# Kernel optimization log

Measured on AMD Instinct MI355X. Metric: run time of the kernel, lower is better.

The kernel has to match this reference:

```python
import jax, jax.numpy as jnp
import numpy as np

ALPHA = 0.8          # triple vs qualifier mixing weight (StarE/QUAD 'sum' strategy)
NUM_ENT = 200000
NUM_REL = 100        # base relations; with inverses rel table has 2*NUM_REL rows
E_DIR = 500000       # edges per direction; edge_index has 2*E_DIR columns
NQ_DIR = 400000      # qualifier (rel, ent, edge_id) triples per direction
D = 200              # emb_dim == gcn_dim
B = 4096             # batch of statements
QP = 6               # qualifier pairs per statement -> quals_ix is [B, 2*QP]


def setup_inputs() -> dict:
    key = jax.random.key(0)
    ks = jax.random.split(key, 24)
    f = lambda i, shape: jax.random.normal(ks[i], shape, jnp.float32) * 0.05
    inp = {
        "ent_embs": f(0, (NUM_ENT, D)),
        "rel_embs": f(1, (2 * NUM_REL, D)),
    }
    for j, n in enumerate(["w_in1", "w_out1", "w_loop1", "w_rel1", "w_q1",
                           "w_in2", "w_out2", "w_loop2", "w_rel2", "w_q2"]):
        inp[n] = f(2 + j, (D, D))
    inp["loop_rel1"] = f(12, (1, D))
    inp["loop_rel2"] = f(13, (1, D))
    inp["b1"] = jnp.zeros((D,), jnp.float32)
    inp["b2"] = jnp.zeros((D,), jnp.float32)
    src = jax.random.randint(ks[14], (E_DIR,), 0, NUM_ENT)
    dst = jax.random.randint(ks[15], (E_DIR,), 0, NUM_ENT)
    # second half are inverse edges
    inp["edge_index"] = jnp.concatenate([jnp.stack([src, dst]), jnp.stack([dst, src])], axis=1)
    et = jax.random.randint(ks[16], (E_DIR,), 0, NUM_REL)
    inp["edge_type"] = jnp.concatenate([et, et + NUM_REL])
    q_r = jax.random.randint(ks[17], (2 * NQ_DIR,), 0, 2 * NUM_REL)
    q_e = jax.random.randint(ks[18], (2 * NQ_DIR,), 0, NUM_ENT)
    q_eid = jax.random.randint(ks[19], (2 * NQ_DIR,), 0, E_DIR)
    inp["quals"] = jnp.stack([q_r, q_e, q_eid])  # [3, 2*NQ_DIR]
    inp["ent_ix"] = jax.random.randint(ks[20], (B,), 0, NUM_ENT)
    inp["rel_ix"] = jax.random.randint(ks[21], (B,), 0, 2 * NUM_REL)
    qi_r = jax.random.randint(ks[22], (B, QP), 0, 2 * NUM_REL)
    qi_e = jax.random.randint(ks[23], (B, QP), 0, NUM_ENT)
    inp["quals_ix"] = jnp.stack([qi_r, qi_e], axis=-1).reshape(B, 2 * QP)  # alternating rel, ent
    return inp


def _comp(h, r):  # CompGCN 'mult' composition
    return h * r


def _compgcn_conv(x, r, edge_index, edge_type, quals,
                  w_in, w_out, w_loop, w_rel, w_q, loop_rel, bias):
    n_ent = x.shape[0]
    E = edge_index.shape[1] // 2
    NQ = quals.shape[1] // 2
    rel_all = jnp.concatenate([r, loop_rel], axis=0)  # loop relation appended last

    def one_dir(idx, etype, q_r, q_e, q_eid, w):
        src, dst = idx[0], idx[1]
        # qualifier-aware per-edge relation embedding
        q_msg = _comp(x[q_e], rel_all[q_r])                               # [NQ, d]
        q_agg = jax.ops.segment_sum(q_msg, q_eid, num_segments=E)        # scatter-sum onto edges
        rel_e = ALPHA * rel_all[etype] + (1.0 - ALPHA) * (q_agg @ w_q)   # [E, d]
        msg = _comp(x[src], rel_e) @ w                                   # [E, d_out]
        deg = jax.ops.segment_sum(jnp.ones((E,), x.dtype), src, num_segments=n_ent)
        dinv = jnp.where(deg > 0, jax.lax.rsqrt(jnp.maximum(deg, 1.0)), 0.0)
        norm = dinv[src] * dinv[dst]                                     # sym degree norm
        return jax.ops.segment_sum(norm[:, None] * msg, dst, num_segments=n_ent)

    in_res = one_dir(edge_index[:, :E], edge_type[:E],
                     quals[0, :NQ], quals[1, :NQ], quals[2, :NQ], w_in)
    out_res = one_dir(edge_index[:, E:], edge_type[E:],
                      quals[0, NQ:], quals[1, NQ:], quals[2, NQ:], w_out)
    loop_res = _comp(x, loop_rel) @ w_loop
    out = (in_res + out_res + loop_res) / 3.0 + bias
    return jnp.tanh(out), rel_all[:-1] @ w_rel


def reference(ent_embs, rel_embs,
              w_in1, w_out1, w_loop1, w_rel1, w_q1, loop_rel1, b1,
              w_in2, w_out2, w_loop2, w_rel2, w_q2, loop_rel2, b2,
              edge_index, edge_type, quals, ent_ix, rel_ix, quals_ix):
    x, r = _compgcn_conv(ent_embs, rel_embs, edge_index, edge_type, quals,
                         w_in1, w_out1, w_loop1, w_rel1, w_q1, loop_rel1, b1)
    x, r = _compgcn_conv(x, r, edge_index, edge_type, quals,
                         w_in2, w_out2, w_loop2, w_rel2, w_q2, loop_rel2, b2)
    sub_emb = x[ent_ix]                                   # [B, d]
    rel_emb = r[rel_ix]                                   # [B, d]
    quals_ents = quals_ix[:, 1::2].reshape(-1)
    quals_rels = quals_ix[:, 0::2].reshape(-1)
    qual_obj_emb = x[quals_ents].reshape(sub_emb.shape[0], -1, sub_emb.shape[1])
    qual_rel_emb = r[quals_rels].reshape(rel_emb.shape[0], -1, rel_emb.shape[1])
    return (sub_emb, rel_emb, qual_obj_emb, qual_rel_emb, x, r)
```

## Files before the change

kernel.cpp:

```cpp
#include <hip/hip_runtime.h>
#include <cstdio>


#define ALPHA_MIX 0.8f

constexpr int N_ENT  = 200000;
constexpr int D_     = 200;
constexpr int E_DIR_ = 500000;
constexpr int NQ_    = 400000;
constexpr int B_     = 4096;

constexpr int NT_  = 13;
constexpr int LDA_ = 232;
constexpr int WLD_ = 224;
constexpr int SB_  = 232;
constexpr int PB_  = 80;
constexpr int NTILES_ = (N_ENT + 15) / 16;

constexpr size_t OFS_SUB  = 0;
constexpr size_t OFS_REL  = 819200;
constexpr size_t OFS_QOBJ = 1638400;
constexpr size_t OFS_QREL = 6553600;
constexpr size_t OFS_X    = 11468800;
constexpr size_t OFS_R    = 51468800;

typedef __bf16 bf16x8 __attribute__((ext_vector_type(8)));
typedef float  f32x4  __attribute__((ext_vector_type(4)));

__device__ __forceinline__ unsigned int f2bf(float f) {
  unsigned int u = __float_as_uint(f);
  u += 0x7FFFu + ((u >> 16) & 1u);
  return u >> 16;
}
__device__ __forceinline__ unsigned long long pack4bf(float x, float y, float z, float w) {
  return (unsigned long long)f2bf(x) | ((unsigned long long)f2bf(y) << 16) |
         ((unsigned long long)f2bf(z) << 32) | ((unsigned long long)f2bf(w) << 48);
}
__device__ __forceinline__ float bf_lo(unsigned int u) { return __uint_as_float(u << 16); }
__device__ __forceinline__ float bf_hi(unsigned int u) { return __uint_as_float(u & 0xFFFF0000u); }
__device__ __forceinline__ unsigned int mulpk(unsigned int a, unsigned int b) {
  return f2bf(bf_lo(a) * bf_lo(b)) | (f2bf(bf_hi(a) * bf_hi(b)) << 16);
}
__device__ __forceinline__ float fast_tanh(float x) {
  float xx = fminf(fmaxf(x, -9.0f), 9.0f);
  float e = __builtin_amdgcn_exp2f(xx * 2.8853900817779268f);
  return (e - 1.0f) * __builtin_amdgcn_rcpf(e + 1.0f);
}

typedef short v2s __attribute__((ext_vector_type(2)));
__device__ __forceinline__ void atomic_pk_add_bf16(unsigned short* addr, unsigned int pk) {
#if __has_builtin(__builtin_amdgcn_global_atomic_fadd_v2bf16)
  v2s v;
  __builtin_memcpy(&v, &pk, 4);
  __builtin_amdgcn_global_atomic_fadd_v2bf16(
      (__attribute__((address_space(1))) v2s*)(unsigned long long)addr, v);
#else
  unsigned int* ap = (unsigned int*)addr;
  unsigned int old = *ap;
  while (true) {
    unsigned int nv = f2bf(bf_lo(old) + bf_lo(pk)) | (f2bf(bf_hi(old) + bf_hi(pk)) << 16);
    unsigned int prev = atomicCAS(ap, old, nv);
    if (prev == old) break;
    old = prev;
  }
#endif
}

__global__ __launch_bounds__(256)
void gemm_qual(const unsigned short* __restrict__ Xbf, const unsigned short* __restrict__ Rbf,
               const int* __restrict__ q_e, const int* __restrict__ q_r,
               const int* __restrict__ q_eid,
               const int* __restrict__ srcv, const int* __restrict__ dstv,
               const float* __restrict__ nrm,
               const unsigned short* __restrict__ Bp,
               unsigned short* __restrict__ pre, int nrows)
{
  __shared__ __align__(16) unsigned short As[64 * LDA_];
  __shared__ int s_g[64], s_r[64], s_eid[64], s_dst[64];
  __shared__ float s_nm[64];

  const int t  = threadIdx.x;
  const int r0 = blockIdx.x * 64;

  if (t < 64) {
    int cr = min(r0 + t, nrows - 1);
    s_g[t] = q_e[cr]; s_r[t] = q_r[cr]; s_eid[t] = q_eid[cr];
  }
  __syncthreads();

  for (int task = t; task < 64 * 25; task += 256) {
    int i = task / 25, c = task % 25;
    uint4 xv = ((const uint4*)(Xbf + (size_t)s_g[i] * D_))[c];
    uint4 rv = ((const uint4*)(Rbf + (size_t)s_r[i] * D_))[c];
    uint4 o;
    o.x = mulpk(xv.x, rv.x); o.y = mulpk(xv.y, rv.y);
    o.z = mulpk(xv.z, rv.z); o.w = mulpk(xv.w, rv.w);
    *(uint4*)(As + i * LDA_ + c * 8) = o;
  }
  for (int task = t; task < 64 * 3; task += 256) {
    int i = task / 3, c = task % 3;
    *(uint4*)(As + i * LDA_ + 200 + c * 8) = make_uint4(0, 0, 0, 0);
  }
  __syncthreads();

  const int wave = t >> 6, lane = t & 63;
  const int m = lane & 15, quad = lane >> 4;

  f32x4 acc[NT_];
  const f32x4 zero = {0.f, 0.f, 0.f, 0.f};
  #pragma unroll
  for (int i = 0; i < NT_; i++) acc[i] = zero;

  {
    const unsigned short* arow = As + (wave * 16 + m) * LDA_ + quad * 8;
    const unsigned short* brow = Bp + (size_t)m * WLD_ + quad * 8;
    #pragma unroll
    for (int ks = 0; ks < 7; ks++) {
      bf16x8 av = *(const bf16x8*)(arow + ks * 32);
      #pragma unroll
      for (int tt = 0; tt < NT_; tt++) {
        bf16x8 bv = *(const bf16x8*)(brow + (size_t)tt * 16 * WLD_ + ks * 32);
        acc[tt] = __builtin_amdgcn_mfma_f32_16x16x32_bf16(av, bv, acc[tt], 0, 0, 0);
      }
    }
  }

  __syncthreads();
  if (t < 64) {
    int e = s_eid[t];
    s_dst[t] = dstv[e];
    s_nm[t]  = (1.0f - ALPHA_MIX) * nrm[e];
    s_g[t]   = srcv[e];
  }
  __syncthreads();
  for (int task = t; task < 64 * 25; task += 256) {
    int i = task / 25, c = task % 25;
    *(uint4*)(As + i * LDA_ + c * 8) = ((const uint4*)(Xbf + (size_t)s_g[i] * D_))[c];
  }
  __syncthreads();

  #pragma unroll
  for (int rg = 0; rg < 4; rg++) {
    int row = r0 + wave * 16 + quad * 4 + rg;
    bool valid = row < nrows;
    int li = row - r0;
    size_t orow = (size_t)s_dst[li] * D_;
    float nm = s_nm[li];
    #pragma unroll
    for (int tt = 0; tt < NT_; tt++) {
      int col = tt * 16 + m;
      float xv = (col < D_) ? __uint_as_float(((unsigned int)As[li * LDA_ + col]) << 16) : 0.0f;
      float v  = acc[tt][rg] * nm * xv;
      float vn = __shfl_xor(v, 1);
      if (valid && !(m & 1) && col < D_) {
        unsigned int pk = f2bf(v) | (f2bf(vn) << 16);
        atomic_pk_add_bf16(pre + orow + col, pk);
      }
    }
  }
}

__global__ __launch_bounds__(256)
void node_gather(const int* __restrict__ starts, const int* __restrict__ csr,
                 const int* __restrict__ srcv, const int* __restrict__ et,
                 const float* __restrict__ nrm,
                 const unsigned short* __restrict__ xbf,
                 const unsigned short* __restrict__ rallbf,
                 unsigned short* __restrict__ pre)
{
  int node = blockIdx.x * 4 + (threadIdx.x >> 6);
  if (node >= N_ENT) return;
  int lane = threadIdx.x & 63;
  int p0 = starts[node], p1 = starts[node + 1];
  float a0 = 0.f, a1 = 0.f, a2 = 0.f, a3 = 0.f;
  for (int p = p0; p < p1; p++) {
    int e = csr[p];
    int s = srcv[e], ty = et[e];
    float nm = nrm[e];
    if (lane < 50) {
      uint2 xv = ((const uint2*)(xbf + (size_t)s * D_))[lane];
      uint2 rv = ((const uint2*)(rallbf + (size_t)ty * D_))[lane];
      a0 += nm * bf_lo(xv.x) * bf_lo(rv.x);
      a1 += nm * bf_hi(xv.x) * bf_hi(rv.x);
      a2 += nm * bf_lo(xv.y) * bf_lo(rv.y);
      a3 += nm * bf_hi(xv.y) * bf_hi(rv.y);
    }
  }
  if (lane < 50) {
    uint2 o;
    o.x = f2bf(a0 * ALPHA_MIX) | (f2bf(a1 * ALPHA_MIX) << 16);
    o.y = f2bf(a2 * ALPHA_MIX) | (f2bf(a3 * ALPHA_MIX) << 16);
    ((uint2*)(pre + (size_t)node * D_))[lane] = o;
  }
}

template<int NTH>
__device__ __forceinline__ void node_core(
    const unsigned short* Bl,
    const unsigned short* __restrict__ pre0,
    const unsigned short* __restrict__ pre1,
    const unsigned short* __restrict__ xsrc,
    const uint4* lv,
    const float* __restrict__ bias,
    float* __restrict__ xo, unsigned short* __restrict__ xbo,
    int rowblk, int wave, int m, int quad, int ncol0, int nrows)
{
  for (int i = wave; i < 49; i += 8) {
    int T = rowblk * 49 + i;
    if (T >= NTILES_) break;
    int rowi = min(T * 16 + m, nrows - 1);
    const unsigned short* a0 = pre0 + (size_t)rowi * D_ + quad * 8;
    const unsigned short* a1 = pre1 + (size_t)rowi * D_ + quad * 8;
    const unsigned short* a2 = xsrc + (size_t)rowi * D_ + quad * 8;

    uint4 af[3][7];
    #pragma unroll
    for (int ks = 0; ks < 7; ks++) af[0][ks] = *(const uint4*)(a0 + ks * 32);
    #pragma unroll
    for (int ks = 0; ks < 7; ks++) af[1][ks] = *(const uint4*)(a1 + ks * 32);
    #pragma unroll
    for (int ks = 0; ks < 7; ks++) af[2][ks] = *(const uint4*)(a2 + ks * 32);

    f32x4 acc[NTH];
    const f32x4 zero = {0.f, 0.f, 0.f, 0.f};
    #pragma unroll
    for (int tt = 0; tt < NTH; tt++) acc[tt] = zero;

    #pragma unroll
    for (int seg = 0; seg < 3; seg++) {
      #pragma unroll
      for (int ks = 0; ks < 7; ks++) {
        uint4 a = af[seg][ks];
        if (seg == 2) {
          a.x = mulpk(a.x, lv[ks].x); a.y = mulpk(a.y, lv[ks].y);
          a.z = mulpk(a.z, lv[ks].z); a.w = mulpk(a.w, lv[ks].w);
        }
        bf16x8 av; __builtin_memcpy(&av, &a, 16);
        #pragma unroll
        for (int tt = 0; tt < NTH; tt++) {
          const unsigned short* bp = Bl + (size_t)(seg * PB_ + tt * 16 + m) * SB_ + quad * 8 + ks * 32;
          bf16x8 bv = *(const bf16x8*)bp;
          acc[tt] = __builtin_amdgcn_mfma_f32_16x16x32_bf16(av, bv, acc[tt], 0, 0, 0);
        }
      }
    }

    #pragma unroll
    for (int rg = 0; rg < 4; rg++) {
      int row = T * 16 + quad * 4 + rg;
      if (row < nrows) {
        #pragma unroll
        for (int tt = 0; tt < NTH; tt++) {
          int col = ncol0 + tt * 16 + m;
          if (col < D_) {
            float v = acc[tt][rg] * (1.0f / 3.0f) + bias[col];
            float th = fast_tanh(v);
            if (xo)  xo[(size_t)row * D_ + col] = th;
            if (xbo) xbo[(size_t)row * D_ + col] = (unsigned short)f2bf(th);
          }
        }
      }
    }
  }
}

__global__ __launch_bounds__(512)
void gemm_node(const unsigned short* __restrict__ pre0,
               const unsigned short* __restrict__ pre1,
               const unsigned short* __restrict__ xsrc,
               const unsigned short* __restrict__ lrel,
               const unsigned short* __restrict__ B0,
               const unsigned short* __restrict__ B1,
               const unsigned short* __restrict__ B2,
               const float* __restrict__ bias,
               float* __restrict__ xo, unsigned short* __restrict__ xbo,
               int nrows)
{
  __shared__ __align__(16) unsigned short Bl[3 * PB_ * SB_];
  const int t   = threadIdx.x;
  const int bid = blockIdx.x;
  const int x8 = bid & 7, q = bid >> 3;
  const int part   = q % 3;
  const int rowblk = (q / 3) * 8 + x8;
  const int nth    = (part == 2) ? 3 : 5;
  const int ncol0  = part * PB_;
  const int nrB    = nth * 16;

  const unsigned short* Bs[3] = {B0, B1, B2};
  for (int task = t; task < 3 * nrB * 28; task += 512) {
    int seg = task / (nrB * 28);
    int rem = task % (nrB * 28);
    int n = rem / 28, c = rem % 28;
    uint4 v = *(const uint4*)(Bs[seg] + (size_t)(ncol0 + n) * WLD_ + c * 8);
    *(uint4*)(Bl + (size_t)(seg * PB_ + n) * SB_ + c * 8) = v;
  }
  __syncthreads();

  const int wave = t >> 6, lane = t & 63;
  const int m = lane & 15, quad = lane >> 4;

  uint4 lv[7];
  #pragma unroll
  for (int ks = 0; ks < 7; ks++)
    lv[ks] = *(const uint4*)(lrel + quad * 8 + ks * 32);

  if (part == 2)
    node_core<3>(Bl, pre0, pre1, xsrc, lv, bias, xo, xbo, rowblk, wave, m, quad, ncol0, nrows);
  else
    node_core<5>(Bl, pre0, pre1, xsrc, lv, bias, xo, xbo, rowblk, wave, m, quad, ncol0, nrows);
}

__global__ __launch_bounds__(256)
void gemm_rel200(const float* __restrict__ X, const unsigned short* __restrict__ Bp,
                 float* __restrict__ Out, int nrows)
{
  __shared__ __align__(16) unsigned short As[64 * LDA_];
  const int t  = threadIdx.x;
  const int r0 = blockIdx.x * 64;

  for (int task = t; task < 64 * 50; task += 256) {
    int i = task / 50, c = task % 50;
    int cr = min(r0 + i, nrows - 1);
    float4 xv = ((const float4*)(X + (size_t)cr * D_))[c];
    *(unsigned long long*)&As[i * LDA_ + c * 4] = pack4bf(xv.x, xv.y, xv.z, xv.w);
  }
  for (int task = t; task < 64 * 6; task += 256) {
    int i = task / 6, c = task % 6;
    *(unsigned long long*)&As[i * LDA_ + 200 + c * 4] = 0ull;
  }
  __syncthreads();

  const int wave = t >> 6, lane = t & 63;
  const int m = lane & 15, quad = lane >> 4;

  f32x4 acc[NT_];
  const f32x4 zero = {0.f, 0.f, 0.f, 0.f};
  #pragma unroll
  for (int i = 0; i < NT_; i++) acc[i] = zero;

  const unsigned short* arow = As + (wave * 16 + m) * LDA_ + quad * 8;
  const unsigned short* brow = Bp + (size_t)m * WLD_ + quad * 8;
  #pragma unroll
  for (int ks = 0; ks < 7; ks++) {
    bf16x8 av = *(const bf16x8*)(arow + ks * 32);
    #pragma unroll
    for (int tt = 0; tt < NT_; tt++) {
      bf16x8 bv = *(const bf16x8*)(brow + (size_t)tt * 16 * WLD_ + ks * 32);
      acc[tt] = __builtin_amdgcn_mfma_f32_16x16x32_bf16(av, bv, acc[tt], 0, 0, 0);
    }
  }

  #pragma unroll
  for (int rg = 0; rg < 4; rg++) {
    int row = r0 + wave * 16 + quad * 4 + rg;
    if (row < nrows) {
      #pragma unroll
      for (int tt = 0; tt < NT_; tt++) {
        int col = tt * 16 + m;
        if (col < D_) Out[(size_t)row * D_ + col] = acc[tt][rg];
      }
    }
  }
}

struct WP10 { const float* p[10]; };

__global__ void convert_weights(WP10 wp, unsigned short* __restrict__ wbp) {
  int i = blockIdx.x * 256 + threadIdx.x;
  if (i < 10 * 208 * WLD_) {
    int j = i / (208 * WLD_);
    int rem = i % (208 * WLD_);
    int n = rem / WLD_, k = rem % WLD_;
    float v = (n < D_ && k < D_) ? wp.p[j][(size_t)k * D_ + n] : 0.0f;
    wbp[i] = (unsigned short)f2bf(v);
  }
}

__global__ void conv_f32_bf16_vec(const float* __restrict__ src,
                                  unsigned short* __restrict__ dst, int n4) {
  int i = blockIdx.x * 256 + threadIdx.x;
  if (i < n4) {
    float4 v = ((const float4*)src)[i];
    uint2 o;
    o.x = f2bf(v.x) | (f2bf(v.y) << 16);
    o.y = f2bf(v.z) | (f2bf(v.w) << 16);
    ((uint2*)dst)[i] = o;
  }
}

__global__ void build_rall(const float* __restrict__ rel_embs,
                           const float* __restrict__ loop_rel,
                           float* __restrict__ rall) {
  int i = blockIdx.x * 256 + threadIdx.x;
  if (i < 201 * D_) rall[i] = (i < 200 * D_) ? rel_embs[i] : loop_rel[i - 200 * D_];
}

__global__ void copy_row(const float* __restrict__ src, float* __restrict__ dst, int n) {
  int i = blockIdx.x * 256 + threadIdx.x;
  if (i < n) dst[i] = src[i];
}

__global__ void deg_count(const int* __restrict__ src, int* __restrict__ deg, int E) {
  int e = blockIdx.x * 256 + threadIdx.x;
  if (e < E) atomicAdd(&deg[src[e]], 1);
}

__global__ void norm_build(const int* __restrict__ src, const int* __restrict__ dst,
                           const int* __restrict__ deg, float* __restrict__ nrm, int E) {
  int e = blockIdx.x * 256 + threadIdx.x;
  if (e < E) {
    int a = deg[src[e]], b = deg[dst[e]];
    float fa = (a > 0) ? rsqrtf((float)a) : 0.0f;
    float fb = (b > 0) ? rsqrtf((float)b) : 0.0f;
    nrm[e] = fa * fb;
  }
}

constexpr int SCHUNK = 2048;

__global__ void scan_partial(const int* __restrict__ in, int* __restrict__ part, int n) {
  __shared__ int red[256];
  int b = blockIdx.x, t = threadIdx.x;
  int base = b * SCHUNK + t * 8;
  int s = 0;
  #pragma unroll
  for (int j = 0; j < 8; j++) { int i = base + j; if (i < n) s += in[i]; }
  red[t] = s; __syncthreads();
  for (int off = 128; off > 0; off >>= 1) {
    if (t < off) red[t] += red[t + off];
    __syncthreads();
  }
  if (t == 0) part[b] = red[0];
}

__global__ void scan_part_seq(int* part, int nb) {
  if (threadIdx.x == 0 && blockIdx.x == 0) {
    int run = 0;
    for (int i = 0; i < nb; i++) { int v = part[i]; part[i] = run; run += v; }
  }
}

__global__ void scan_final(const int* __restrict__ in, const int* __restrict__ part,
                           int* __restrict__ outs, int* __restrict__ cursor,
                           int n, int total) {
  __shared__ int buf[256];
  int b = blockIdx.x, t = threadIdx.x;
  int base = b * SCHUNK + t * 8;
  int v[8]; int s = 0;
  #pragma unroll
  for (int j = 0; j < 8; j++) { int i = base + j; v[j] = (i < n) ? in[i] : 0; s += v[j]; }
  buf[t] = s; __syncthreads();
  for (int off = 1; off < 256; off <<= 1) {
    int add = (t >= off) ? buf[t - off] : 0;
    __syncthreads();
    buf[t] += add;
    __syncthreads();
  }
  int excl = buf[t] - s + part[b];
  #pragma unroll
  for (int j = 0; j < 8; j++) {
    int i = base + j;
    if (i < n) { outs[i] = excl; cursor[i] = excl; }
    excl += v[j];
  }
  if (b == 0 && t == 0) outs[n] = total;
}

__global__ void fill_csr(const int* __restrict__ dstv, int* __restrict__ cursor,
                         int* __restrict__ csr, int E) {
  int e = blockIdx.x * 256 + threadIdx.x;
  if (e < E) {
    int pos = atomicAdd(&cursor[dstv[e]], 1);
    csr[pos] = e;
  }
}

__global__ void gather_out(const float* __restrict__ x2, const float* __restrict__ r2,
                           const int* __restrict__ ent_ix, const int* __restrict__ rel_ix,
                           const int* __restrict__ quals_ix, float* __restrict__ out) {
  int i = blockIdx.x * 256 + threadIdx.x;
  if (i >= B_ * 14 * 50) return;
  int b = i / 700, rem = i % 700, slot = rem / 50, c = rem % 50;
  const float* srcrow; float* dstrow;
  if (slot == 0)      { srcrow = x2 + (size_t)ent_ix[b] * D_;  dstrow = out + OFS_SUB + (size_t)b * D_; }
  else if (slot == 1) { srcrow = r2 + (size_t)rel_ix[b] * D_;  dstrow = out + OFS_REL + (size_t)b * D_; }
  else if (slot < 8)  { int j = slot - 2;
                        srcrow = x2 + (size_t)quals_ix[b * 12 + 2 * j + 1] * D_;
                        dstrow = out + OFS_QOBJ + ((size_t)b * 6 + j) * D_; }
  else                { int j = slot - 8;
                        srcrow = r2 + (size_t)quals_ix[b * 12 + 2 * j] * D_;
                        dstrow = out + OFS_QREL + ((size_t)b * 6 + j) * D_; }
  ((float4*)dstrow)[c] = ((const float4*)srcrow)[c];
}

extern "C" void kernel_launch(void* const* d_in, const int* in_sizes, int n_in,
                              void* d_out, int out_size, void* d_ws, size_t ws_size,
                              hipStream_t stream)
{
  const float* ent       = (const float*)d_in[0];
  const float* rel_embs  = (const float*)d_in[1];
  const float* loop_rel1 = (const float*)d_in[12];
  const float* loop_rel2 = (const float*)d_in[13];
  const float* b1        = (const float*)d_in[14];
  const float* b2        = (const float*)d_in[15];
  const int*   ei        = (const int*)d_in[16];
  const int*   etype     = (const int*)d_in[17];
  const int*   quals     = (const int*)d_in[18];
  const int*   ent_ix    = (const int*)d_in[19];
  const int*   rel_ix    = (const int*)d_in[20];
  const int*   quals_ix  = (const int*)d_in[21];

  char* wsb = (char*)d_ws;
  size_t off = 0;
  auto walloc = [&](size_t bytes) -> char* {
    char* p = wsb + off; off += (bytes + 511) & ~(size_t)511; return p;
  };
  unsigned short* pre0  = (unsigned short*)walloc((size_t)N_ENT * D_ * 2);
  unsigned short* pre1  = (unsigned short*)walloc((size_t)N_ENT * D_ * 2);
  unsigned short* x_bf  = (unsigned short*)walloc((size_t)N_ENT * D_ * 2);
  unsigned short* xb2   = (unsigned short*)walloc((size_t)N_ENT * D_ * 2);
  float* norm1 = (float*)walloc((size_t)E_DIR_ * 4);
  float* norm2 = (float*)walloc((size_t)E_DIR_ * 4);
  int*   degA  = (int*)walloc((size_t)N_ENT * 4);
  int*   degB  = (int*)walloc((size_t)N_ENT * 4);
  int*   starts0 = (int*)walloc((size_t)(N_ENT + 1) * 4);
  int*   starts1 = (int*)walloc((size_t)(N_ENT + 1) * 4);
  int*   cursor0 = (int*)walloc((size_t)N_ENT * 4);
  int*   cursor1 = (int*)walloc((size_t)N_ENT * 4);
  int*   csr0    = (int*)walloc((size_t)E_DIR_ * 4);
  int*   csr1    = (int*)walloc((size_t)E_DIR_ * 4);
  int*   part    = (int*)walloc((size_t)256 * 4);
  float* rall1 = (float*)walloc((size_t)201 * D_ * 4);
  float* rall2 = (float*)walloc((size_t)201 * D_ * 4);
  unsigned short* rall1_bf = (unsigned short*)walloc((size_t)201 * D_ * 2);
  unsigned short* rall2_bf = (unsigned short*)walloc((size_t)201 * D_ * 2);
  unsigned short* lrel1_bf = (unsigned short*)walloc((size_t)D_ * 2);
  unsigned short* lrel2_bf = (unsigned short*)walloc((size_t)D_ * 2);
  unsigned short* wbp = (unsigned short*)walloc((size_t)10 * 208 * WLD_ * 2);
  if (off > ws_size) fprintf(stderr, "ws overflow: need %zu have %zu\n", off, ws_size);

  float* out   = (float*)d_out;
  float* x_out = out + OFS_X;
  float* r_out = out + OFS_R;

  auto WB = [&](int j) { return wbp + (size_t)j * 208 * WLD_; };

  WP10 wp; for (int j = 0; j < 10; j++) wp.p[j] = (const float*)d_in[2 + j];
  convert_weights<<<(10 * 208 * WLD_ + 255) / 256, 256, 0, stream>>>(wp, wbp);
  build_rall<<<(201 * D_ + 255) / 256, 256, 0, stream>>>(rel_embs, loop_rel1, rall1);
  conv_f32_bf16_vec<<<(201 * 50 + 255) / 256, 256, 0, stream>>>(rall1, rall1_bf, 201 * 50);
  conv_f32_bf16_vec<<<(N_ENT * 50 + 255) / 256, 256, 0, stream>>>(ent, x_bf, N_ENT * 50);
  conv_f32_bf16_vec<<<1, 256, 0, stream>>>(loop_rel1, lrel1_bf, 50);
  conv_f32_bf16_vec<<<1, 256, 0, stream>>>(loop_rel2, lrel2_bf, 50);

  const int* src1 = ei;
  const int* dst1 = ei + 2 * E_DIR_;
  const int* src2 = ei + E_DIR_;
  const int* dst2 = ei + 3 * E_DIR_;

  int gE = (E_DIR_ + 255) / 256;
  hipMemsetAsync(degA, 0, (size_t)N_ENT * 4, stream);
  hipMemsetAsync(degB, 0, (size_t)N_ENT * 4, stream);
  deg_count<<<gE, 256, 0, stream>>>(src1, degA, E_DIR_);
  deg_count<<<gE, 256, 0, stream>>>(src2, degB, E_DIR_);
  norm_build<<<gE, 256, 0, stream>>>(src1, dst1, degA, norm1, E_DIR_);
  norm_build<<<gE, 256, 0, stream>>>(src2, dst2, degB, norm2, E_DIR_);

  int nbScan = (N_ENT + SCHUNK - 1) / SCHUNK;
  scan_partial<<<nbScan, 256, 0, stream>>>(degB, part, N_ENT);
  scan_part_seq<<<1, 64, 0, stream>>>(part, nbScan);
  scan_final<<<nbScan, 256, 0, stream>>>(degB, part, starts0, cursor0, N_ENT, E_DIR_);
  fill_csr<<<gE, 256, 0, stream>>>(dst1, cursor0, csr0, E_DIR_);

  scan_partial<<<nbScan, 256, 0, stream>>>(degA, part, N_ENT);
  scan_part_seq<<<1, 64, 0, stream>>>(part, nbScan);
  scan_final<<<nbScan, 256, 0, stream>>>(degA, part, starts1, cursor1, N_ENT, E_DIR_);
  fill_csr<<<gE, 256, 0, stream>>>(dst2, cursor1, csr1, E_DIR_);

  const int* q_r   = quals;
  const int* q_e   = quals + 2 * NQ_;
  const int* q_eid = quals + 4 * NQ_;

  for (int layer = 0; layer < 2; layer++) {
    const float* rallf = layer ? rall2 : rall1;
    const unsigned short* rallbf = layer ? rall2_bf : rall1_bf;
    const unsigned short* lrelbf = layer ? lrel2_bf : lrel1_bf;
    const float* bias = layer ? b2 : b1;
    const unsigned short* w_q    = WB(layer ? 9 : 4);
    const unsigned short* w_loop = WB(layer ? 7 : 2);
    const unsigned short* w_rel  = WB(layer ? 8 : 3);
    const unsigned short* w_in   = WB(layer ? 5 : 0);
    const unsigned short* w_out  = WB(layer ? 6 : 1);
    const unsigned short* xin    = layer ? xb2 : x_bf;

    float* r_dst = layer ? r_out : rall2;
    gemm_rel200<<<4, 256, 0, stream>>>(rallf, w_rel, r_dst, 200);
    if (layer == 0) {
      copy_row<<<1, 256, 0, stream>>>(loop_rel2, rall2 + (size_t)200 * D_, D_);
      conv_f32_bf16_vec<<<(201 * 50 + 255) / 256, 256, 0, stream>>>(rall2, rall2_bf, 201 * 50);
    }

    for (int dir = 0; dir < 2; dir++) {
      const int* et  = etype + dir * E_DIR_;
      const int* qr  = q_r + dir * NQ_;
      const int* qe  = q_e + dir * NQ_;
      const int* qid = q_eid + dir * NQ_;
      const int* s   = dir ? src2 : src1;
      const int* dd  = dir ? dst2 : dst1;
      const float* nm = dir ? norm2 : norm1;
      const int* sts = dir ? starts1 : starts0;
      const int* csr = dir ? csr1 : csr0;
      unsigned short* pre = dir ? pre1 : pre0;

      node_gather<<<(N_ENT + 3) / 4, 256, 0, stream>>>(sts, csr, s, et, nm, xin, rallbf, pre);
      gemm_qual<<<(NQ_ + 63) / 64, 256, 0, stream>>>(xin, rallbf, qe, qr, qid,
                                                     s, dd, nm, w_q, pre, NQ_);
    }

    if (layer == 0)
      gemm_node<<<768, 512, 0, stream>>>(pre0, pre1, xin, lrelbf,
                                         w_in, w_out, w_loop, bias,
                                         (float*)nullptr, xb2, N_ENT);
    else
      gemm_node<<<768, 512, 0, stream>>>(pre0, pre1, xin, lrelbf,
                                         w_in, w_out, w_loop, bias,
                                         x_out, (unsigned short*)nullptr, N_ENT);
  }

  gather_out<<<(B_ * 14 * 50 + 255) / 256, 256, 0, stream>>>(
      x_out, r_out, ent_ix, rel_ix, quals_ix, out);
}
```

Baseline: 2.962 ms.

## Aggregate qualifiers per edge before projection and fold into gather, removing atomics

Builds a per-edge CSR of qualifiers and a compacted list of edges that have qualifiers. The qualifier GEMM now first sums the x*r products per edge and multiplies each covered edge by w_q once, writing a dense per-edge result. The node gather then mixes that result into the relation term, which removes the scattered bf16 atomic adds into the pre-activation buffer. This adds preprocessing scans, an extra workspace buffer and an extra read per edge in the gather.

```diff
diff --git a/kernel.cpp b/kernel.cpp
--- a/kernel.cpp
+++ b/kernel.cpp
@@ -47,54 +47,44 @@
   return (e - 1.0f) * __builtin_amdgcn_rcpf(e + 1.0f);
 }
 
-typedef short v2s __attribute__((ext_vector_type(2)));
-__device__ __forceinline__ void atomic_pk_add_bf16(unsigned short* addr, unsigned int pk) {
-#if __has_builtin(__builtin_amdgcn_global_atomic_fadd_v2bf16)
-  v2s v;
-  __builtin_memcpy(&v, &pk, 4);
-  __builtin_amdgcn_global_atomic_fadd_v2bf16(
-      (__attribute__((address_space(1))) v2s*)(unsigned long long)addr, v);
-#else
-  unsigned int* ap = (unsigned int*)addr;
-  unsigned int old = *ap;
-  while (true) {
-    unsigned int nv = f2bf(bf_lo(old) + bf_lo(pk)) | (f2bf(bf_hi(old) + bf_hi(pk)) << 16);
-    unsigned int prev = atomicCAS(ap, old, nv);
-    if (prev == old) break;
-    old = prev;
-  }
-#endif
-}
-
 __global__ __launch_bounds__(256)
-void gemm_qual(const unsigned short* __restrict__ Xbf, const unsigned short* __restrict__ Rbf,
-               const int* __restrict__ q_e, const int* __restrict__ q_r,
-               const int* __restrict__ q_eid,
-               const int* __restrict__ srcv, const int* __restrict__ dstv,
-               const float* __restrict__ nrm,
-               const unsigned short* __restrict__ Bp,
-               unsigned short* __restrict__ pre, int nrows)
+void gemm_qedge(const unsigned short* __restrict__ Xbf, const unsigned short* __restrict__ Rbf,
+                const int* __restrict__ q_e, const int* __restrict__ q_r,
+                const int* __restrict__ qstarts, const int* __restrict__ qcsr,
+                const int* __restrict__ covlist, const int* __restrict__ ncovp,
+                const unsigned short* __restrict__ Bp,
+                unsigned short* __restrict__ y)
 {
   __shared__ __align__(16) unsigned short As[64 * LDA_];
-  __shared__ int s_g[64], s_r[64], s_eid[64], s_dst[64];
-  __shared__ float s_nm[64];
-
-  const int t  = threadIdx.x;
+  __shared__ int s_p0[64], s_p1[64];
+
+  const int ncov = ncovp[0];
   const int r0 = blockIdx.x * 64;
+  if (r0 >= ncov) return;
+  const int t = threadIdx.x;
 
   if (t < 64) {
-    int cr = min(r0 + t, nrows - 1);
-    s_g[t] = q_e[cr]; s_r[t] = q_r[cr]; s_eid[t] = q_eid[cr];
+    int ce = r0 + t;
+    if (ce < ncov) { int e = covlist[ce]; s_p0[t] = qstarts[e]; s_p1[t] = qstarts[e + 1]; }
+    else           { s_p0[t] = 0; s_p1[t] = 0; }
   }
   __syncthreads();
 
   for (int task = t; task < 64 * 25; task += 256) {
     int i = task / 25, c = task % 25;
-    uint4 xv = ((const uint4*)(Xbf + (size_t)s_g[i] * D_))[c];
-    uint4 rv = ((const uint4*)(Rbf + (size_t)s_r[i] * D_))[c];
+    float a0=0,a1=0,a2=0,a3=0,a4=0,a5=0,a6=0,a7=0;
+    for (int p = s_p0[i]; p < s_p1[i]; p++) {
+      int q = qcsr[p];
+      uint4 xv = ((const uint4*)(Xbf + (size_t)q_e[q] * D_))[c];
+      uint4 rv = ((const uint4*)(Rbf + (size_t)q_r[q] * D_))[c];
+      a0 += bf_lo(xv.x) * bf_lo(rv.x); a1 += bf_hi(xv.x) * bf_hi(rv.x);
+      a2 += bf_lo(xv.y) * bf_lo(rv.y); a3 += bf_hi(xv.y) * bf_hi(rv.y);
+      a4 += bf_lo(xv.z) * bf_lo(rv.z); a5 += bf_hi(xv.z) * bf_hi(rv.z);
+      a6 += bf_lo(xv.w) * bf_lo(rv.w); a7 += bf_hi(xv.w) * bf_hi(rv.w);
+    }
     uint4 o;
-    o.x = mulpk(xv.x, rv.x); o.y = mulpk(xv.y, rv.y);
-    o.z = mulpk(xv.z, rv.z); o.w = mulpk(xv.w, rv.w);
+    o.x = f2bf(a0) | (f2bf(a1) << 16); o.y = f2bf(a2) | (f2bf(a3) << 16);
+    o.z = f2bf(a4) | (f2bf(a5) << 16); o.w = f2bf(a6) | (f2bf(a7) << 16);
     *(uint4*)(As + i * LDA_ + c * 8) = o;
   }
   for (int task = t; task < 64 * 3; task += 256) {
@@ -125,36 +115,17 @@
     }
   }
 
-  __syncthreads();
-  if (t < 64) {
-    int e = s_eid[t];
-    s_dst[t] = dstv[e];
-    s_nm[t]  = (1.0f - ALPHA_MIX) * nrm[e];
-    s_g[t]   = srcv[e];
-  }
-  __syncthreads();
-  for (int task = t; task < 64 * 25; task += 256) {
-    int i = task / 25, c = task % 25;
-    *(uint4*)(As + i * LDA_ + c * 8) = ((const uint4*)(Xbf + (size_t)s_g[i] * D_))[c];
-  }
-  __syncthreads();
-
   #pragma unroll
   for (int rg = 0; rg < 4; rg++) {
     int row = r0 + wave * 16 + quad * 4 + rg;
-    bool valid = row < nrows;
-    int li = row - r0;
-    size_t orow = (size_t)s_dst[li] * D_;
-    float nm = s_nm[li];
+    bool valid = row < ncov;
     #pragma unroll
     for (int tt = 0; tt < NT_; tt++) {
       int col = tt * 16 + m;
-      float xv = (col < D_) ? __uint_as_float(((unsigned int)As[li * LDA_ + col]) << 16) : 0.0f;
-      float v  = acc[tt][rg] * nm * xv;
+      float v  = acc[tt][rg];
       float vn = __shfl_xor(v, 1);
       if (valid && !(m & 1) && col < D_) {
-        unsigned int pk = f2bf(v) | (f2bf(vn) << 16);
-        atomic_pk_add_bf16(pre + orow + col, pk);
+        *(unsigned int*)(y + (size_t)row * D_ + col) = f2bf(v) | (f2bf(vn) << 16);
       }
     }
   }
@@ -164,6 +135,7 @@
 void node_gather(const int* __restrict__ starts, const int* __restrict__ csr,
                  const int* __restrict__ srcv, const int* __restrict__ et,
                  const float* __restrict__ nrm,
+                 const int* __restrict__ qidx, const unsigned short* __restrict__ y,
                  const unsigned short* __restrict__ xbf,
                  const unsigned short* __restrict__ rallbf,
                  unsigned short* __restrict__ pre)
@@ -175,21 +147,30 @@
   float a0 = 0.f, a1 = 0.f, a2 = 0.f, a3 = 0.f;
   for (int p = p0; p < p1; p++) {
     int e = csr[p];
-    int s = srcv[e], ty = et[e];
+    int s = srcv[e], ty = et[e], qi = qidx[e];
     float nm = nrm[e];
     if (lane < 50) {
       uint2 xv = ((const uint2*)(xbf + (size_t)s * D_))[lane];
       uint2 rv = ((const uint2*)(rallbf + (size_t)ty * D_))[lane];
-      a0 += nm * bf_lo(xv.x) * bf_lo(rv.x);
-      a1 += nm * bf_hi(xv.x) * bf_hi(rv.x);
-      a2 += nm * bf_lo(xv.y) * bf_lo(rv.y);
-      a3 += nm * bf_hi(xv.y) * bf_hi(rv.y);
+      float c0 = ALPHA_MIX * bf_lo(rv.x), c1 = ALPHA_MIX * bf_hi(rv.x);
+      float c2 = ALPHA_MIX * bf_lo(rv.y), c3 = ALPHA_MIX * bf_hi(rv.y);
+      if (qi >= 0) {
+        uint2 yv = ((const uint2*)(y + (size_t)qi * D_))[lane];
+        c0 = fmaf(1.0f - ALPHA_MIX, bf_lo(yv.x), c0);
+        c1 = fmaf(1.0f - ALPHA_MIX, bf_hi(yv.x), c1);
+        c2 = fmaf(1.0f - ALPHA_MIX, bf_lo(yv.y), c2);
+        c3 = fmaf(1.0f - ALPHA_MIX, bf_hi(yv.y), c3);
+      }
+      a0 = fmaf(nm * bf_lo(xv.x), c0, a0);
+      a1 = fmaf(nm * bf_hi(xv.x), c1, a1);
+      a2 = fmaf(nm * bf_lo(xv.y), c2, a2);
+      a3 = fmaf(nm * bf_hi(xv.y), c3, a3);
     }
   }
   if (lane < 50) {
     uint2 o;
-    o.x = f2bf(a0 * ALPHA_MIX) | (f2bf(a1 * ALPHA_MIX) << 16);
-    o.y = f2bf(a2 * ALPHA_MIX) | (f2bf(a3 * ALPHA_MIX) << 16);
+    o.x = f2bf(a0) | (f2bf(a1) << 16);
+    o.y = f2bf(a2) | (f2bf(a3) << 16);
     ((uint2*)(pre + (size_t)node * D_))[lane] = o;
   }
 }
@@ -475,6 +456,26 @@
   }
 }
 
+__global__ void mk_flag(const int* __restrict__ deg, int* __restrict__ flag, int n) {
+  int i = blockIdx.x * 256 + threadIdx.x;
+  if (i < n) flag[i] = (deg[i] > 0) ? 1 : 0;
+}
+
+__global__ void fill_cov(const int* __restrict__ flag, const int* __restrict__ covstarts,
+                         int* __restrict__ covlist, int* __restrict__ qidx, int n) {
+  int e = blockIdx.x * 256 + threadIdx.x;
+  if (e < n) {
+    if (flag[e]) { int p = covstarts[e]; covlist[p] = e; qidx[e] = p; }
+    else qidx[e] = -1;
+  }
+}
+
+__global__ void finalize_cov(const int* __restrict__ covstarts, const int* __restrict__ flag,
+                             int* __restrict__ ncovp) {
+  if (threadIdx.x == 0 && blockIdx.x == 0)
+    ncovp[0] = covstarts[E_DIR_ - 1] + flag[E_DIR_ - 1];
+}
+
 __global__ void gather_out(const float* __restrict__ x2, const float* __restrict__ r2,
                            const int* __restrict__ ent_ix, const int* __restrict__ rel_ix,
                            const int* __restrict__ quals_ix, float* __restrict__ out) {
@@ -519,6 +520,7 @@
   unsigned short* pre1  = (unsigned short*)walloc((size_t)N_ENT * D_ * 2);
   unsigned short* x_bf  = (unsigned short*)walloc((size_t)N_ENT * D_ * 2);
   unsigned short* xb2   = (unsigned short*)walloc((size_t)N_ENT * D_ * 2);
+  unsigned short* yq    = (unsigned short*)walloc((size_t)NQ_ * D_ * 2);
   float* norm1 = (float*)walloc((size_t)E_DIR_ * 4);
   float* norm2 = (float*)walloc((size_t)E_DIR_ * 4);
   int*   degA  = (int*)walloc((size_t)N_ENT * 4);
@@ -530,6 +532,20 @@
   int*   csr0    = (int*)walloc((size_t)E_DIR_ * 4);
   int*   csr1    = (int*)walloc((size_t)E_DIR_ * 4);
   int*   part    = (int*)walloc((size_t)256 * 4);
+  int*   qstarts0 = (int*)walloc((size_t)(E_DIR_ + 1) * 4);
+  int*   qstarts1 = (int*)walloc((size_t)(E_DIR_ + 1) * 4);
+  int*   qcsr0    = (int*)walloc((size_t)NQ_ * 4);
+  int*   qcsr1    = (int*)walloc((size_t)NQ_ * 4);
+  int*   covlist0 = (int*)walloc((size_t)E_DIR_ * 4);
+  int*   covlist1 = (int*)walloc((size_t)E_DIR_ * 4);
+  int*   qidx0    = (int*)walloc((size_t)E_DIR_ * 4);
+  int*   qidx1    = (int*)walloc((size_t)E_DIR_ * 4);
+  int*   ncov0p   = (int*)walloc(64);
+  int*   ncov1p   = (int*)walloc(64);
+  int*   qdegS    = (int*)walloc((size_t)E_DIR_ * 4);
+  int*   flagS    = (int*)walloc((size_t)E_DIR_ * 4);
+  int*   qcurS    = (int*)walloc((size_t)E_DIR_ * 4);
+  int*   covstS   = (int*)walloc((size_t)(E_DIR_ + 1) * 4);
   float* rall1 = (float*)walloc((size_t)201 * D_ * 4);
   float* rall2 = (float*)walloc((size_t)201 * D_ * 4);
   unsigned short* rall1_bf = (unsigned short*)walloc((size_t)201 * D_ * 2);
@@ -580,6 +596,31 @@
   const int* q_r   = quals;
   const int* q_e   = quals + 2 * NQ_;
   const int* q_eid = quals + 4 * NQ_;
+
+  int gNQ = (NQ_ + 255) / 256;
+  int nbE = (E_DIR_ + SCHUNK - 1) / SCHUNK;
+  for (int dir = 0; dir < 2; dir++) {
+    const int* qid = q_eid + dir * NQ_;
+    int* qst = dir ? qstarts1 : qstarts0;
+    int* qcs = dir ? qcsr1 : qcsr0;
+    int* cvl = dir ? covlist1 : covlist0;
+    int* qix = dir ? qidx1 : qidx0;
+    int* ncv = dir ? ncov1p : ncov0p;
+
+    hipMemsetAsync(qdegS, 0, (size_t)E_DIR_ * 4, stream);
+    deg_count<<<gNQ, 256, 0, stream>>>(qid, qdegS, NQ_);
+    scan_partial<<<nbE, 256, 0, stream>>>(qdegS, part, E_DIR_);
+    scan_part_seq<<<1, 64, 0, stream>>>(part, nbE);
+    scan_final<<<nbE, 256, 0, stream>>>(qdegS, part, qst, qcurS, E_DIR_, NQ_);
+    fill_csr<<<gNQ, 256, 0, stream>>>(qid, qcurS, qcs, NQ_);
+
+    mk_flag<<<gE, 256, 0, stream>>>(qdegS, flagS, E_DIR_);
+    scan_partial<<<nbE, 256, 0, stream>>>(flagS, part, E_DIR_);
+    scan_part_seq<<<1, 64, 0, stream>>>(part, nbE);
+    scan_final<<<nbE, 256, 0, stream>>>(flagS, part, covstS, qcurS, E_DIR_, 0);
+    fill_cov<<<gE, 256, 0, stream>>>(flagS, covstS, cvl, qix, E_DIR_);
+    finalize_cov<<<1, 64, 0, stream>>>(covstS, flagS, ncv);
+  }
 
   for (int layer = 0; layer < 2; layer++) {
     const float* rallf = layer ? rall2 : rall1;
@@ -602,19 +643,23 @@
 
     for (int dir = 0; dir < 2; dir++) {
       const int* et  = etype + dir * E_DIR_;
+      const int* qe  = q_e + dir * NQ_;
       const int* qr  = q_r + dir * NQ_;
-      const int* qe  = q_e + dir * NQ_;
-      const int* qid = q_eid + dir * NQ_;
       const int* s   = dir ? src2 : src1;
-      const int* dd  = dir ? dst2 : dst1;
       const float* nm = dir ? norm2 : norm1;
       const int* sts = dir ? starts1 : starts0;
       const int* csr = dir ? csr1 : csr0;
+      const int* qst = dir ? qstarts1 : qstarts0;
+      const int* qcs = dir ? qcsr1 : qcsr0;
+      const int* cvl = dir ? covlist1 : covlist0;
+      const int* qix = dir ? qidx1 : qidx0;
+      const int* ncv = dir ? ncov1p : ncov0p;
       unsigned short* pre = dir ? pre1 : pre0;
 
-      node_gather<<<(N_ENT + 3) / 4, 256, 0, stream>>>(sts, csr, s, et, nm, xin, rallbf, pre);
-      gemm_qual<<<(NQ_ + 63) / 64, 256, 0, stream>>>(xin, rallbf, qe, qr, qid,
-                                                     s, dd, nm, w_q, pre, NQ_);
+      gemm_qedge<<<(NQ_ + 63) / 64, 256, 0, stream>>>(xin, rallbf, qe, qr,
+                                                      qst, qcs, cvl, ncv, w_q, yq);
+      node_gather<<<(N_ENT + 3) / 4, 256, 0, stream>>>(sts, csr, s, et, nm,
+                                                       qix, yq, xin, rallbf, pre);
     }
 
     if (layer == 0)
```

Result: faster. 2.766 ms (-6.6%).
